# Kernel tuning notes

Measured on AMD Instinct MI355X. Metric: run time of the kernel, lower is better.

## Reference

```python
import jax, jax.numpy as jnp
import numpy as np

HIDDEN = 4096
N_HEADS = 32
N_KV_HEADS = 8
HEAD_DIM = HIDDEN // N_HEADS  # 128
ROPE_THETA = 500000.0
B, S = 1, 2048


def setup_inputs() -> dict:
    key = jax.random.key(0)
    k1, k2, k3, k4, k5 = jax.random.split(key, 5)
    scale = 0.02
    return {
        "hidden_states": jax.random.normal(k1, (B, S, HIDDEN), dtype=jnp.float32),
        "Wq": jax.random.normal(k2, (N_HEADS * HEAD_DIM, HIDDEN), dtype=jnp.float32) * scale,
        "Wk": jax.random.normal(k3, (N_KV_HEADS * HEAD_DIM, HIDDEN), dtype=jnp.float32) * scale,
        "Wv": jax.random.normal(k4, (N_KV_HEADS * HEAD_DIM, HIDDEN), dtype=jnp.float32) * scale,
        "Wo": jax.random.normal(k5, (HIDDEN, N_HEADS * HEAD_DIM), dtype=jnp.float32) * scale,
    }


def _rope_cos_sin(seq_len, head_dim, theta, dtype):
    inv_freq = 1.0 / (theta ** (jnp.arange(0, head_dim, 2, dtype=jnp.float32) / head_dim))  # [hd/2]
    pos = jnp.arange(seq_len, dtype=jnp.float32)
    freqs = jnp.outer(pos, inv_freq)                      # [S, hd/2]
    emb = jnp.concatenate([freqs, freqs], axis=-1)        # [S, hd]
    return jnp.cos(emb).astype(dtype), jnp.sin(emb).astype(dtype)


def _rotate_half(x):
    x1, x2 = jnp.split(x, 2, axis=-1)
    return jnp.concatenate([-x2, x1], axis=-1)


def _apply_rope(x, cos, sin):
    # x: [B, H, S, hd]; cos/sin: [S, hd]
    return x * cos[None, None] + _rotate_half(x) * sin[None, None]


def reference(hidden_states, Wq, Wk, Wv, Wo):
    b, s, _ = hidden_states.shape
    groups = N_HEADS // N_KV_HEADS

    # fused QKV projections (Linear with weight [out, in])
    q = jnp.einsum("bsd,ed->bse", hidden_states, Wq).reshape(b, s, N_HEADS, HEAD_DIM).transpose(0, 2, 1, 3)
    k = jnp.einsum("bsd,ed->bse", hidden_states, Wk).reshape(b, s, N_KV_HEADS, HEAD_DIM).transpose(0, 2, 1, 3)
    v = jnp.einsum("bsd,ed->bse", hidden_states, Wv).reshape(b, s, N_KV_HEADS, HEAD_DIM).transpose(0, 2, 1, 3)

    cos, sin = _rope_cos_sin(s, HEAD_DIM, ROPE_THETA, hidden_states.dtype)
    q = _apply_rope(q, cos, sin)
    k = _apply_rope(k, cos, sin)

    # GQA: repeat kv heads across groups
    k = jnp.repeat(k, groups, axis=1)  # [B, N_HEADS, S, hd]
    v = jnp.repeat(v, groups, axis=1)

    scale = 1.0 / jnp.sqrt(jnp.asarray(HEAD_DIM, dtype=hidden_states.dtype))
    scores = jnp.einsum("bhqd,bhkd->bhqk", q, k) * scale  # [B, H, S, S]
    causal = jnp.tril(jnp.ones((s, s), dtype=bool))
    scores = jnp.where(causal[None, None], scores, jnp.asarray(-1e30, dtype=scores.dtype))
    attn = jax.nn.softmax(scores, axis=-1)

    out = jnp.einsum("bhqk,bhkd->bhqd", attn, v)          # [B, H, S, hd]
    out = out.transpose(0, 2, 1, 3).reshape(b, s, N_HEADS * HEAD_DIM)
    return jnp.einsum("bse,de->bsd", out, Wo)             # [B, S, HIDDEN]
```

## Files before the change

kernel.cpp:

```cpp
#include <hip/hip_runtime.h>

typedef __attribute__((ext_vector_type(8))) short bf16x8;
typedef __attribute__((ext_vector_type(4))) short bf16x4;
typedef __attribute__((ext_vector_type(4))) float f32x4;
typedef __attribute__((ext_vector_type(16))) float f32x16;

#define S_LEN  2048
#define HID    4096
#define NHEADS 32
#define NKVH   8
#define HDIM   128
#define QKVN   (HID + 2*NKVH*HDIM)
#define KOFS   HID
#define VOFS   (HID + NKVH*HDIM)

#define AS1 __attribute__((address_space(1)))
#define AS3 __attribute__((address_space(3)))

__device__ __forceinline__ unsigned short f2bf(float f){
  unsigned int x = __float_as_uint(f);
  x += 0x7fffu + ((x >> 16) & 1u);
  return (unsigned short)(x >> 16);
}
__device__ __forceinline__ float bf2f(unsigned short h){
  return __uint_as_float(((unsigned int)h) << 16);
}

__global__ void cvt_all(const float* __restrict__ hs, const float* __restrict__ wq,
                        const float* __restrict__ wk, const float* __restrict__ wv,
                        const float* __restrict__ wo,
                        unsigned short* __restrict__ Hb,
                        unsigned short* __restrict__ Wqkvb,
                        unsigned short* __restrict__ Wob){
  const int total = 12582912;
  for (int i = blockIdx.x * blockDim.x + threadIdx.x; i < total; i += gridDim.x * blockDim.x){
    const float* src; unsigned short* dst;
    if (i < 2097152)      { src = hs + (size_t)i*4;             dst = Hb    + (size_t)i*4; }
    else if (i < 6291456) { size_t l = i - 2097152;  src = wq + l*4; dst = Wqkvb + l*4; }
    else if (i < 7340032) { size_t l = i - 6291456;  src = wk + l*4; dst = Wqkvb + 16777216 + l*4; }
    else if (i < 8388608) { size_t l = i - 7340032;  src = wv + l*4; dst = Wqkvb + 20971520 + l*4; }
    else                  { size_t l = i - 8388608;  src = wo + l*4; dst = Wob   + l*4; }
    float4 v = *(const float4*)src;
    ushort4 o;
    o.x = f2bf(v.x); o.y = f2bf(v.y); o.z = f2bf(v.z); o.w = f2bf(v.w);
    *(ushort4*)dst = o;
  }
}

__global__ void rope_table(float* __restrict__ cosT, float* __restrict__ sinT){
  int idx = blockIdx.x * blockDim.x + threadIdx.x;
  int s = idx >> 6, i = idx & 63;
  float inv = expf(-(float)i * (13.122363377404329f / 64.0f));
  float a = (float)s * inv;
  cosT[idx] = cosf(a);
  sinT[idx] = sinf(a);
}

__global__ void rope_apply(unsigned short* __restrict__ X, const float* __restrict__ cosT,
                           const float* __restrict__ sinT, int nh, int rowstr, int colofs, int total){
  int idx = blockIdx.x * blockDim.x + threadIdx.x;
  if (idx >= total) return;
  int i = idx & 63;
  int h = (idx >> 6) % nh;
  int s = idx / (64*nh);
  size_t base = (size_t)s*rowstr + colofs + h*HDIM + i;
  float x0 = bf2f(X[base]), x1 = bf2f(X[base+64]);
  float c = cosT[(s<<6)|i], sn = sinT[(s<<6)|i];
  X[base]    = f2bf(x0*c - x1*sn);
  X[base+64] = f2bf(x1*c + x0*sn);
}

__global__ __launch_bounds__(256) void transpose_v(const unsigned short* __restrict__ QKV,
                                                   unsigned short* __restrict__ Vt){
  __shared__ unsigned short T[64][130];
  const int qt = blockIdx.x, kvh = blockIdx.y;
  const int tid = threadIdx.x;
  #pragma unroll
  for (int i=0;i<4;i++){
    int c = tid + i*256;
    int sl = c >> 4;
    int d0 = (c & 15) * 8;
    bf16x8 v = *(const bf16x8*)&QKV[(size_t)(qt*64+sl)*QKVN + VOFS + kvh*HDIM + d0];
    #pragma unroll
    for (int j=0;j<8;j++) T[sl][d0+j] = (unsigned short)v[j];
  }
  __syncthreads();
  #pragma unroll
  for (int i=0;i<4;i++){
    int c = tid + i*256;
    int d = c >> 3;
    int p0 = (c & 7) * 8;
    bf16x8 o;
    #pragma unroll
    for (int j=0;j<8;j++) o[j] = (short)T[p0+j][d];
    *(bf16x8*)&Vt[((size_t)kvh*HDIM + d)*S_LEN + qt*64 + p0] = o;
  }
}

template<int BM, int BN, int OUTF32>
__global__ __launch_bounds__(512, 2) void gemm_fr(const unsigned short* __restrict__ A,
                                                  const unsigned short* __restrict__ W,
                                                  void* __restrict__ C, int M, int N, int K){
  constexpr int MF = BM/32;
  constexpr int NF = BN/64;
  constexpr int LA = BM/64;
  constexpr int LB = BN/64;
  constexpr int ABYTES = BM*128;
  constexpr int BBYTES = BN*128;
  __shared__ char lds_raw[2*ABYTES + 2*BBYTES];

  const int tid = threadIdx.x;
  const int lane = tid & 63, wv = tid >> 6;
  const int wm = wv >> 2, wn = wv & 3;
  const int r = lane & 15, kq = lane >> 4;
  const int tn = blockIdx.x, tm = blockIdx.y;
  const unsigned short* Ab = A + (size_t)tm*BM*K;
  const unsigned short* Wb = W + (size_t)tn*BN*K;

  f32x4 acc[MF][NF];
  #pragma unroll
  for (int m=0;m<MF;m++)
    #pragma unroll
    for (int n=0;n<NF;n++) acc[m][n] = {0.f,0.f,0.f,0.f};

  auto swz = [](int row)->int { return ((row>>1)&3)<<1; };

  auto stage = [&](int buf, int kt){
    #pragma unroll
    for (int l=0;l<LA;l++){
      int c = l*512 + tid;
      int row = c >> 3, ch = c & 7;
      __builtin_amdgcn_global_load_lds(
        (const AS1 void*)(Ab + (size_t)row*K + kt + ((ch ^ swz(row))*8)),
        (AS3 void*)(lds_raw + buf*ABYTES + (l*512 + wv*64)*16), 16, 0, 0);
    }
    #pragma unroll
    for (int l=0;l<LB;l++){
      int c = l*512 + tid;
      int row = c >> 3, ch = c & 7;
      __builtin_amdgcn_global_load_lds(
        (const AS1 void*)(Wb + (size_t)row*K + kt + ((ch ^ swz(row))*8)),
        (AS3 void*)(lds_raw + 2*ABYTES + buf*BBYTES + (l*512 + wv*64)*16), 16, 0, 0);
    }
  };
  auto rdA = [&](int buf, int m, int kh)->bf16x8 {
    int row = wm*(BM/2) + m*16 + r;
    int ch = (kh*4 + kq) ^ swz(row);
    return *(const bf16x8*)(lds_raw + buf*ABYTES + row*128 + ch*16);
  };
  auto rdB = [&](int buf, int n, int kh)->bf16x8 {
    int row = wn*(BN/4) + n*16 + r;
    int ch = (kh*4 + kq) ^ swz(row);
    return *(const bf16x8*)(lds_raw + 2*ABYTES + buf*BBYTES + row*128 + ch*16);
  };

  const int nt = K/64;
  stage(0, 0);
  for (int t=0; t<nt; ++t){
    asm volatile("s_waitcnt vmcnt(0)" ::: "memory");
    __builtin_amdgcn_s_barrier();
    if (t+1 < nt) stage((t+1)&1, (t+1)*64);
    const int buf = t & 1;
    #pragma unroll
    for (int kh=0; kh<2; ++kh){
      bf16x8 av[MF], bv[NF];
      #pragma unroll
      for (int m=0;m<MF;m++) av[m] = rdA(buf, m, kh);
      #pragma unroll
      for (int n=0;n<NF;n++) bv[n] = rdB(buf, n, kh);
      #pragma unroll
      for (int m=0;m<MF;m++)
        #pragma unroll
        for (int n=0;n<NF;n++)
          acc[m][n] = __builtin_amdgcn_mfma_f32_16x16x32_bf16(av[m], bv[n], acc[m][n], 0, 0, 0);
    }
  }

  #pragma unroll
  for (int m=0;m<MF;m++)
    #pragma unroll
    for (int n=0;n<NF;n++)
      #pragma unroll
      for (int j=0;j<4;j++){
        int gr = tm*BM + wm*(BM/2) + m*16 + kq*4 + j;
        int gc = tn*BN + wn*(BN/4) + n*16 + r;
        if (OUTF32) ((float*)C)[(size_t)gr*N + gc] = acc[m][n][j];
        else ((unsigned short*)C)[(size_t)gr*N + gc] = f2bf(acc[m][n][j]);
      }
}

__global__ __launch_bounds__(256, 2) void attn_fwd3(const unsigned short* __restrict__ QKV,
                                                    const unsigned short* __restrict__ Vt,
                                                    unsigned short* __restrict__ AO){
  __shared__ unsigned short Ks[2][64*128];
  __shared__ unsigned short Vs[2][128*64];
  __shared__ float Ls[4][32];
  const int tid = threadIdx.x;
  const int lane = tid & 63, wv = tid >> 6;
  const int bid = blockIdx.x;
  const int h = bid & 31;
  const int qt = (S_LEN/128 - 1) - (bid >> 5);
  const int kvh = h >> 2;
  const int qb = qt * 128;
  const int q0w = qb + wv * 32;
  const int l31 = lane & 31, g = lane >> 5;
  const int qg = q0w + l31;

  const float CS = 0.12751743f;
  const float C0 = 17.312340f;

  bf16x8 qf[8];
  #pragma unroll
  for (int st=0; st<8; ++st)
    qf[st] = *(const bf16x8*)&QKV[(size_t)qg*QKVN + h*HDIM + st*16 + g*8];

  f32x16 oacc[4];
  #pragma unroll
  for (int db=0; db<4; ++db)
    #pragma unroll
    for (int i=0;i<16;i++) oacc[db][i] = 0.f;
  float lsum = 0.f;

  const unsigned short* Kbase = QKV + KOFS + kvh*HDIM;
  const unsigned short* Vbase = Vt + (size_t)kvh*HDIM*S_LEN;

  auto stage = [&](int buf, int kv0){
    #pragma unroll
    for (int l=0; l<4; ++l){
      int c = l*256 + tid;
      int row = c >> 4, ch = c & 15;
      __builtin_amdgcn_global_load_lds(
        (const AS1 void*)(Kbase + (size_t)(kv0+row)*QKVN + ((ch ^ (row&15))*8)),
        (AS3 void*)((char*)&Ks[buf][0] + (l*256 + wv*64)*16), 16, 0, 0);
    }
    #pragma unroll
    for (int l=0; l<4; ++l){
      int c = l*256 + tid;
      int row = c >> 3, ch = c & 7;
      __builtin_amdgcn_global_load_lds(
        (const AS1 void*)(Vbase + (size_t)row*S_LEN + kv0 + ((ch ^ (row&7))*8)),
        (AS3 void*)((char*)&Vs[buf][0] + (l*256 + wv*64)*16), 16, 0, 0);
    }
  };

  const int nt = 2*qt + 2;
  stage(0, 0);
  for (int t=0; t<nt; ++t){
    __syncthreads();
    if (t+1 < nt) stage((t+1)&1, (t+1)*64);
    const int kv0 = t*64;
    if (kv0 > q0w + 31) continue;
    const unsigned short* K_ = &Ks[t&1][0];
    const unsigned short* V_ = &Vs[t&1][0];

    f32x16 a0, a1;
    #pragma unroll
    for (int i=0;i<16;i++){ a0[i]=0.f; a1[i]=0.f; }
    #pragma unroll
    for (int st=0; st<8; ++st){
      int ch = (2*st + g) ^ (l31 & 15);
      bf16x8 k0 = *(const bf16x8*)&K_[ l31*128      + ch*8 ];
      int ch1 = (2*st + g) ^ ((32+l31) & 15);
      bf16x8 k1 = *(const bf16x8*)&K_[ (32+l31)*128 + ch1*8 ];
      a0 = __builtin_amdgcn_mfma_f32_32x32x16_bf16(k0, qf[st], a0, 0,0,0);
      a1 = __builtin_amdgcn_mfma_f32_32x32x16_bf16(k1, qf[st], a1, 0,0,0);
    }

    float p0[16], p1[16];
    const bool dm = (kv0 + 63 > q0w);
    const int lim = qg - kv0 - 4*g;
    #pragma unroll
    for (int i=0;i<16;i++){
      const int co = (i&3) + 8*(i>>2);
      float e0 = fmaf(a0[i], CS, -C0);
      float e1 = fmaf(a1[i], CS, -C0);
      if (dm){
        if (co      > lim) e0 = -200.f;
        if (co + 32 > lim) e1 = -200.f;
      }
      p0[i] = exp2f(fminf(e0, 60.f));
      p1[i] = exp2f(fminf(e1, 60.f));
    }
    {
      float u0 = (p0[0]+p0[1])+(p0[2]+p0[3]);
      float u1 = (p0[4]+p0[5])+(p0[6]+p0[7]);
      float u2 = (p0[8]+p0[9])+(p0[10]+p0[11]);
      float u3 = (p0[12]+p0[13])+(p0[14]+p0[15]);
      float v0 = (p1[0]+p1[1])+(p1[2]+p1[3]);
      float v1 = (p1[4]+p1[5])+(p1[6]+p1[7]);
      float v2 = (p1[8]+p1[9])+(p1[10]+p1[11]);
      float v3 = (p1[12]+p1[13])+(p1[14]+p1[15]);
      lsum += ((u0+u1)+(u2+u3)) + ((v0+v1)+(v2+v3));
    }

    bf16x8 pa[4];
    #pragma unroll
    for (int u=0; u<4; ++u){
      const float* P = (u<2) ? p0 : p1;
      const int i0 = 8*(u&1);
      unsigned int w0,w1,w2,w3;
      asm("v_cvt_pk_bf16_f32 %0, %1, %2" : "=v"(w0) : "v"(P[i0+0]), "v"(P[i0+1]));
      asm("v_cvt_pk_bf16_f32 %0, %1, %2" : "=v"(w1) : "v"(P[i0+2]), "v"(P[i0+3]));
      asm("v_cvt_pk_bf16_f32 %0, %1, %2" : "=v"(w2) : "v"(P[i0+4]), "v"(P[i0+5]));
      asm("v_cvt_pk_bf16_f32 %0, %1, %2" : "=v"(w3) : "v"(P[i0+6]), "v"(P[i0+7]));
      unsigned int r0 = __shfl_xor(g ? w0 : w2, 32);
      unsigned int r1 = __shfl_xor(g ? w1 : w3, 32);
      union { unsigned int u4[4]; bf16x8 v; } pk;
      pk.u4[0] = g ? r0 : w0;
      pk.u4[1] = g ? r1 : w1;
      pk.u4[2] = g ? w2 : r0;
      pk.u4[3] = g ? w3 : r1;
      pa[u] = pk.v;
    }

    #pragma unroll
    for (int u=0; u<4; ++u)
      #pragma unroll
      for (int db=0; db<4; ++db){
        int row = db*32 + l31;
        int ch = (2*u + g) ^ (row & 7);
        bf16x8 vb = *(const bf16x8*)&V_[row*64 + ch*8];
        oacc[db] = __builtin_amdgcn_mfma_f32_32x32x16_bf16(pa[u], vb, oacc[db], 0,0,0);
      }
  }

  float ls = lsum + __shfl_xor(lsum, 32);
  float inv = 1.0f / fmaxf(ls, 1e-30f);
  Ls[wv][l31] = inv;
  #pragma unroll
  for (int ib=0; ib<4; ++ib){
    float4 iv = *(const float4*)&Ls[wv][8*ib + 4*g];
    float ivv[4] = {iv.x, iv.y, iv.z, iv.w};
    #pragma unroll
    for (int c3=0; c3<4; ++c3){
      int row = 8*ib + 4*g + c3;
      #pragma unroll
      for (int db=0; db<4; ++db){
        AO[(size_t)(qb + wv*32 + row)*HID + h*HDIM + db*32 + l31] =
          f2bf(oacc[db][4*ib+c3] * ivv[c3]);
      }
    }
  }
}

extern "C" void kernel_launch(void* const* d_in, const int* in_sizes, int n_in,
                              void* d_out, int out_size, void* d_ws, size_t ws_size,
                              hipStream_t stream){
  (void)in_sizes; (void)n_in; (void)out_size; (void)ws_size;
  const float* hs = (const float*)d_in[0];
  const float* Wq = (const float*)d_in[1];
  const float* Wk = (const float*)d_in[2];
  const float* Wv = (const float*)d_in[3];
  const float* Wo = (const float*)d_in[4];
  float* out = (float*)d_out;
  char* ws = (char*)d_ws;
  size_t off = 0;
  auto alloc = [&](size_t bytes)->void*{ void* p = ws + off; off += (bytes + 255) & ~(size_t)255; return p; };

  unsigned short* Hb    = (unsigned short*)alloc((size_t)S_LEN*HID*2);
  unsigned short* Wqkvb = (unsigned short*)alloc((size_t)QKVN*HID*2);
  unsigned short* Wob   = (unsigned short*)alloc((size_t)HID*HID*2);
  unsigned short* QKVb  = (unsigned short*)alloc((size_t)S_LEN*QKVN*2);
  unsigned short* AOb   = (unsigned short*)alloc((size_t)S_LEN*HID*2);
  unsigned short* Vtb   = (unsigned short*)alloc((size_t)NKVH*HDIM*S_LEN*2);
  float* cosT = (float*)alloc((size_t)S_LEN*64*4);
  float* sinT = (float*)alloc((size_t)S_LEN*64*4);

  cvt_all<<<2048, 256, 0, stream>>>(hs, Wq, Wk, Wv, Wo, Hb, Wqkvb, Wob);
  rope_table<<<(S_LEN*64)/256, 256, 0, stream>>>(cosT, sinT);

  gemm_fr<256,192,0><<<dim3(QKVN/192, S_LEN/256), 512, 0, stream>>>(Hb, Wqkvb, QKVb, S_LEN, QKVN, HID);

  transpose_v<<<dim3(S_LEN/64, NKVH), 256, 0, stream>>>(QKVb, Vtb);

  int totQ = S_LEN*NHEADS*64;
  rope_apply<<<(totQ+255)/256, 256, 0, stream>>>(QKVb, cosT, sinT, NHEADS, QKVN, 0,    totQ);
  int totK = S_LEN*NKVH*64;
  rope_apply<<<(totK+255)/256, 256, 0, stream>>>(QKVb, cosT, sinT, NKVH,   QKVN, KOFS, totK);

  attn_fwd3<<<dim3(512), 256, 0, stream>>>(QKVb, Vtb, AOb);

  gemm_fr<128,256,1><<<dim3(HID/256, S_LEN/128), 512, 0, stream>>>(AOb, Wob, out, S_LEN, HID, HID);
}
```

Before: 299.5 us.

## Retile GEMMs to 256-thread blocks with configurable warp grid; fuse RoPE launches

The GEMM kernel is generalized to a template warp layout (WM x WN) with 256 threads per block instead of 512. The QKV projection now uses 128x192 tiles with a 1x4 warp grid, and the output projection uses 128x128 tiles with a 2x2 grid, giving more blocks and different per-warp fragment counts. The two RoPE launches for Q and K are merged into one kernel. The aim is better occupancy and wave balance across the CUs, at the cost of less operand reuse per block and more global and L2 traffic.

```diff
diff --git a/kernel.cpp b/kernel.cpp
--- a/kernel.cpp
+++ b/kernel.cpp
@@ -56,14 +56,19 @@
   sinT[idx] = sinf(a);
 }
 
-__global__ void rope_apply(unsigned short* __restrict__ X, const float* __restrict__ cosT,
-                           const float* __restrict__ sinT, int nh, int rowstr, int colofs, int total){
+__global__ void rope_apply2(unsigned short* __restrict__ X, const float* __restrict__ cosT,
+                            const float* __restrict__ sinT){
+  const int totQ = S_LEN*NHEADS*64;
+  const int total = totQ + S_LEN*NKVH*64;
   int idx = blockIdx.x * blockDim.x + threadIdx.x;
   if (idx >= total) return;
-  int i = idx & 63;
-  int h = (idx >> 6) % nh;
-  int s = idx / (64*nh);
-  size_t base = (size_t)s*rowstr + colofs + h*HDIM + i;
+  int nh, colofs, local;
+  if (idx < totQ){ nh = NHEADS; colofs = 0;    local = idx; }
+  else           { nh = NKVH;   colofs = KOFS; local = idx - totQ; }
+  int i = local & 63;
+  int h = (local >> 6) % nh;
+  int s = local / (64*nh);
+  size_t base = (size_t)s*QKVN + colofs + h*HDIM + i;
   float x0 = bf2f(X[base]), x1 = bf2f(X[base+64]);
   float c = cosT[(s<<6)|i], sn = sinT[(s<<6)|i];
   X[base]    = f2bf(x0*c - x1*sn);
@@ -97,21 +102,21 @@
   }
 }
 
-template<int BM, int BN, int OUTF32>
-__global__ __launch_bounds__(512, 2) void gemm_fr(const unsigned short* __restrict__ A,
+template<int BM, int BN, int WM, int WN, int OUTF32>
+__global__ __launch_bounds__(256, 2) void gemm_fr(const unsigned short* __restrict__ A,
                                                   const unsigned short* __restrict__ W,
                                                   void* __restrict__ C, int M, int N, int K){
-  constexpr int MF = BM/32;
-  constexpr int NF = BN/64;
-  constexpr int LA = BM/64;
-  constexpr int LB = BN/64;
+  constexpr int MF = (BM/WM)/16;
+  constexpr int NF = (BN/WN)/16;
+  constexpr int LA = BM/32;
+  constexpr int LB = BN/32;
   constexpr int ABYTES = BM*128;
   constexpr int BBYTES = BN*128;
   __shared__ char lds_raw[2*ABYTES + 2*BBYTES];
 
   const int tid = threadIdx.x;
   const int lane = tid & 63, wv = tid >> 6;
-  const int wm = wv >> 2, wn = wv & 3;
+  const int wm = wv / WN, wn = wv % WN;
   const int r = lane & 15, kq = lane >> 4;
   const int tn = blockIdx.x, tm = blockIdx.y;
   const unsigned short* Ab = A + (size_t)tm*BM*K;
@@ -128,28 +133,28 @@
   auto stage = [&](int buf, int kt){
     #pragma unroll
     for (int l=0;l<LA;l++){
-      int c = l*512 + tid;
+      int c = l*256 + tid;
       int row = c >> 3, ch = c & 7;
       __builtin_amdgcn_global_load_lds(
         (const AS1 void*)(Ab + (size_t)row*K + kt + ((ch ^ swz(row))*8)),
-        (AS3 void*)(lds_raw + buf*ABYTES + (l*512 + wv*64)*16), 16, 0, 0);
+        (AS3 void*)(lds_raw + buf*ABYTES + (l*256 + wv*64)*16), 16, 0, 0);
     }
     #pragma unroll
     for (int l=0;l<LB;l++){
-      int c = l*512 + tid;
+      int c = l*256 + tid;
       int row = c >> 3, ch = c & 7;
       __builtin_amdgcn_global_load_lds(
         (const AS1 void*)(Wb + (size_t)row*K + kt + ((ch ^ swz(row))*8)),
-        (AS3 void*)(lds_raw + 2*ABYTES + buf*BBYTES + (l*512 + wv*64)*16), 16, 0, 0);
+        (AS3 void*)(lds_raw + 2*ABYTES + buf*BBYTES + (l*256 + wv*64)*16), 16, 0, 0);
     }
   };
   auto rdA = [&](int buf, int m, int kh)->bf16x8 {
-    int row = wm*(BM/2) + m*16 + r;
+    int row = wm*(BM/WM) + m*16 + r;
     int ch = (kh*4 + kq) ^ swz(row);
     return *(const bf16x8*)(lds_raw + buf*ABYTES + row*128 + ch*16);
   };
   auto rdB = [&](int buf, int n, int kh)->bf16x8 {
-    int row = wn*(BN/4) + n*16 + r;
+    int row = wn*(BN/WN) + n*16 + r;
     int ch = (kh*4 + kq) ^ swz(row);
     return *(const bf16x8*)(lds_raw + 2*ABYTES + buf*BBYTES + row*128 + ch*16);
   };
@@ -182,8 +187,8 @@
     for (int n=0;n<NF;n++)
       #pragma unroll
       for (int j=0;j<4;j++){
-        int gr = tm*BM + wm*(BM/2) + m*16 + kq*4 + j;
-        int gc = tn*BN + wn*(BN/4) + n*16 + r;
+        int gr = tm*BM + wm*(BM/WM) + m*16 + kq*4 + j;
+        int gc = tn*BN + wn*(BN/WN) + n*16 + r;
         if (OUTF32) ((float*)C)[(size_t)gr*N + gc] = acc[m][n][j];
         else ((unsigned short*)C)[(size_t)gr*N + gc] = f2bf(acc[m][n][j]);
       }
@@ -369,16 +374,16 @@
   cvt_all<<<2048, 256, 0, stream>>>(hs, Wq, Wk, Wv, Wo, Hb, Wqkvb, Wob);
   rope_table<<<(S_LEN*64)/256, 256, 0, stream>>>(cosT, sinT);
 
-  gemm_fr<256,192,0><<<dim3(QKVN/192, S_LEN/256), 512, 0, stream>>>(Hb, Wqkvb, QKVb, S_LEN, QKVN, HID);
+  gemm_fr<128,192,1,4,0><<<dim3(QKVN/192, S_LEN/128), 256, 0, stream>>>(Hb, Wqkvb, QKVb, S_LEN, QKVN, HID);
 
   transpose_v<<<dim3(S_LEN/64, NKVH), 256, 0, stream>>>(QKVb, Vtb);
 
-  int totQ = S_LEN*NHEADS*64;
-  rope_apply<<<(totQ+255)/256, 256, 0, stream>>>(QKVb, cosT, sinT, NHEADS, QKVN, 0,    totQ);
-  int totK = S_LEN*NKVH*64;
-  rope_apply<<<(totK+255)/256, 256, 0, stream>>>(QKVb, cosT, sinT, NKVH,   QKVN, KOFS, totK);
+  {
+    int total = S_LEN*NHEADS*64 + S_LEN*NKVH*64;
+    rope_apply2<<<(total+255)/256, 256, 0, stream>>>(QKVb, cosT, sinT);
+  }
 
   attn_fwd3<<<dim3(512), 256, 0, stream>>>(QKVb, Vtb, AOb);
 
-  gemm_fr<128,256,1><<<dim3(HID/256, S_LEN/128), 512, 0, stream>>>(AOb, Wob, out, S_LEN, HID, HID);
-}
+  gemm_fr<128,128,2,2,1><<<dim3(HID/128, S_LEN/128), 256, 0, stream>>>(AOb, Wob, out, S_LEN, HID, HID);
+}
```

Result: no change. 298.7 us (-0.3%).
